# Performance work log

Hardware: AMD Instinct MI355X
Metric: run time of the kernel (lower is better)

Reference implementation:

```python
import jax, jax.numpy as jnp
import numpy as np

N = 100000       # nodes
E = 3200000      # edges (avg degree 32)
IN_F = 256
HID = 256
CLS = 64
LN_EPS = 1e-5


def setup_inputs() -> dict:
    key = jax.random.key(0)
    ks = jax.random.split(key, 8)
    features = jax.random.normal(ks[0], (N, IN_F), jnp.float32)
    src = jax.random.randint(ks[1], (E,), 0, N, dtype=jnp.int32)
    dst = jax.random.randint(ks[2], (E,), 0, N, dtype=jnp.int32)
    glorot = lambda k, sh: jax.random.normal(k, sh, jnp.float32) * np.float32(1.0 / np.sqrt(sh[0]))
    return {
        "features": features, "src": src, "dst": dst,
        "W0": glorot(ks[3], (IN_F, HID)), "b0": jnp.zeros((HID,), jnp.float32),
        "W1": glorot(ks[4], (HID, HID)), "b1": jnp.zeros((HID,), jnp.float32),
        "W2": glorot(ks[5], (HID, CLS)), "b2": jnp.zeros((CLS,), jnp.float32),
    }


def _degrees(src, dst):
    ones = jnp.ones(src.shape[0], jnp.float32)
    deg_out = jnp.maximum(jax.ops.segment_sum(ones, src, num_segments=N), 1.0)
    deg_in = jnpmax = jnp.maximum(jax.ops.segment_sum(ones, dst, num_segments=N), 1.0)
    return deg_out ** -0.5, deg_in ** -0.5


def _graph_conv(h, src, dst, norm_src, norm_dst, W, b, act):
    # DGL GraphConv, norm='both': D_dst^{-1/2} A D_src^{-1/2} X W + b
    h = h * norm_src[:, None]
    agg = jax.ops.segment_sum(h[src], dst, num_segments=N)  # [N, d] scatter-add
    h = agg * norm_dst[:, None]
    h = h @ W + b
    return act(h) if act is not None else h


def _full_layernorm(h):
    # F.layer_norm(h, h.shape): normalize over the ENTIRE tensor, no affine
    mu = jnp.mean(h)
    var = jnp.mean(jnp.square(h - mu))
    return (h - mu) * jax.lax.rsqrt(var + LN_EPS)


def reference(features, src, dst, W0, b0, W1, b1, W2, b2):
    norm_src, norm_dst = _degrees(src, dst)
    h = _graph_conv(features, src, dst, norm_src, norm_dst, W0, b0, jax.nn.relu)
    h = _full_layernorm(h)
    # dropout p=0.0 -> identity
    h = _graph_conv(h, src, dst, norm_src, norm_dst, W1, b1, jax.nn.relu)
    h = _full_layernorm(h)
    h = _graph_conv(h, src, dst, norm_src, norm_dst, W2, b2, None)
    return h
```

## Files before the change

kernel.cpp:

```cpp
#include <hip/hip_runtime.h>
#include <hip/hip_fp16.h>


typedef __attribute__((ext_vector_type(8))) short short8v;
typedef __attribute__((ext_vector_type(4))) float float4v;

struct alignas(8) h4_t { __half2 lo, hi; };

static __device__ __forceinline__ unsigned short f2bf(float x) {
  unsigned int u = __float_as_uint(x);
  unsigned int r = (u + 0x7fffu + ((u >> 16) & 1u)) >> 16;
  return (unsigned short)r;
}
static __device__ __forceinline__ float bf2f(unsigned short h) {
  return __uint_as_float((unsigned int)h << 16);
}
static __device__ __forceinline__ unsigned int f2h2(float a, float b) {
  __half2 h = __floats2half2_rn(a, b);
  return *(unsigned int*)&h;
}
static __device__ __forceinline__ unsigned int bfpack(float a, float b) {
  return (unsigned int)f2bf(a) | ((unsigned int)f2bf(b) << 16);
}

__global__ __launch_bounds__(256) void degrees_k(const int* __restrict__ src,
                                                 const int* __restrict__ dst,
                                                 int* __restrict__ degO,
                                                 int* __restrict__ degI, int E) {
  int e = blockIdx.x * 256 + threadIdx.x;
  if (e < E) {
    atomicAdd(&degO[src[e]], 1);
    atomicAdd(&degI[dst[e]], 1);
  }
}

__global__ __launch_bounds__(256) void norm_k(const int* __restrict__ degO,
                                              const int* __restrict__ degI,
                                              float* __restrict__ ns,
                                              float* __restrict__ nd, int N) {
  int n = blockIdx.x * 256 + threadIdx.x;
  if (n < N) {
    int o = degO[n]; if (o < 1) o = 1;
    int i = degI[n]; if (i < 1) i = 1;
    ns[n] = rsqrtf((float)o);
    nd[n] = rsqrtf((float)i);
  }
}

__global__ __launch_bounds__(256) void scan1_k(const int* __restrict__ in,
                                               int* __restrict__ out,
                                               int* __restrict__ partials, int n) {
  __shared__ int sh[256];
  int t = threadIdx.x;
  int base = blockIdx.x * 2048 + t * 8;
  int v[8];
  int local = 0;
#pragma unroll
  for (int j = 0; j < 8; ++j) {
    int idx = base + j;
    v[j] = (idx < n) ? in[idx] : 0;
    local += v[j];
  }
  sh[t] = local;
  __syncthreads();
  int x = local;
  for (int off = 1; off < 256; off <<= 1) {
    int y = (t >= off) ? sh[t - off] : 0;
    __syncthreads();
    x += y;
    sh[t] = x;
    __syncthreads();
  }
  if (t == 255) partials[blockIdx.x] = x;
  int run = x - local;
#pragma unroll
  for (int j = 0; j < 8; ++j) {
    int idx = base + j;
    if (idx < n) out[idx] = run;
    run += v[j];
  }
}

__global__ void scan2_k(int* partials, int nb) {
  if (threadIdx.x == 0 && blockIdx.x == 0) {
    int run = 0;
    for (int i = 0; i < nb; ++i) { int t = partials[i]; partials[i] = run; run += t; }
  }
}

__global__ __launch_bounds__(256) void scan3_k(int* __restrict__ row_start,
                                               int* __restrict__ cursor,
                                               const int* __restrict__ partials,
                                               int n, int total) {
  int i = blockIdx.x * 256 + threadIdx.x;
  if (i < n) {
    int val = row_start[i] + partials[i >> 11];
    row_start[i] = val;
    cursor[i] = val;
  }
  if (i == 0) row_start[n] = total;
}

__global__ __launch_bounds__(256) void fill_k(const int* __restrict__ src,
                                              const int* __restrict__ dst,
                                              int* __restrict__ cursor,
                                              int* __restrict__ edge_src, int E) {
  int e = blockIdx.x * 256 + threadIdx.x;
  if (e < E) {
    int d = dst[e];
    int pos = atomicAdd(&cursor[d], 1);
    edge_src[pos] = src[e];
  }
}

__global__ __launch_bounds__(256) void prepw_k(const float* __restrict__ W,
                                               unsigned short* __restrict__ Whi,
                                               unsigned short* __restrict__ Wlo,
                                               int K, int csh) {
  int C = 1 << csh;
  int idx = blockIdx.x * 256 + threadIdx.x;
  if (idx >= K * C) return;
  int k = idx >> csh, c = idx & (C - 1);
  float x = W[idx];
  unsigned short h = f2bf(x);
  Whi[c * K + k] = h;
  Wlo[c * K + k] = f2bf(x - bf2f(h));
}

__global__ __launch_bounds__(256) void prescale_h_k(const float* __restrict__ X,
                                                    const float* __restrict__ ns,
                                                    __half* __restrict__ Ah, int N) {
  size_t q = (size_t)blockIdx.x * 256 + threadIdx.x;
  if (q >= (size_t)N * 32) return;
  int row = (int)(q >> 5);
  float s = ns[row];
  float4 v0 = ((const float4*)X)[q * 2];
  float4 v1 = ((const float4*)X)[q * 2 + 1];
  uint4 o;
  o.x = f2h2(v0.x * s, v0.y * s);
  o.y = f2h2(v0.z * s, v0.w * s);
  o.z = f2h2(v1.x * s, v1.y * s);
  o.w = f2h2(v1.z * s, v1.w * s);
  ((uint4*)Ah)[q] = o;
}

__global__ __launch_bounds__(256) void normp_h_k(const float* __restrict__ A,
                                                 const float* __restrict__ ns,
                                                 const double* __restrict__ stats,
                                                 double inv_count,
                                                 __half* __restrict__ Ah, int N) {
  size_t q = (size_t)blockIdx.x * 256 + threadIdx.x;
  if (q >= (size_t)N * 32) return;
  double mu = stats[0] * inv_count;
  double var = stats[1] * inv_count - mu * mu;
  float muf = (float)mu;
  float inv = (float)(1.0 / sqrt(var + 1e-5));
  int row = (int)(q >> 5);
  float sc = ns[row] * inv;
  float4 v0 = ((const float4*)A)[q * 2];
  float4 v1 = ((const float4*)A)[q * 2 + 1];
  uint4 o;
  o.x = f2h2((v0.x - muf) * sc, (v0.y - muf) * sc);
  o.y = f2h2((v0.z - muf) * sc, (v0.w - muf) * sc);
  o.z = f2h2((v1.x - muf) * sc, (v1.y - muf) * sc);
  o.w = f2h2((v1.z - muf) * sc, (v1.w - muf) * sc);
  ((uint4*)Ah)[q] = o;
}

__global__ __launch_bounds__(256) void normp_p_k(const float* __restrict__ A,
                                                 const float* __restrict__ ns,
                                                 const double* __restrict__ stats,
                                                 double inv_count,
                                                 unsigned short* __restrict__ Phi,
                                                 unsigned short* __restrict__ Plo,
                                                 int N) {
  size_t q = (size_t)blockIdx.x * 256 + threadIdx.x;
  if (q >= (size_t)N * 32) return;
  double mu = stats[0] * inv_count;
  double var = stats[1] * inv_count - mu * mu;
  float muf = (float)mu;
  float inv = (float)(1.0 / sqrt(var + 1e-5));
  int row = (int)(q >> 5);
  float sc = ns[row] * inv;
  float x[8];
  float4 v0 = ((const float4*)A)[q * 2];
  float4 v1 = ((const float4*)A)[q * 2 + 1];
  x[0] = (v0.x - muf) * sc; x[1] = (v0.y - muf) * sc;
  x[2] = (v0.z - muf) * sc; x[3] = (v0.w - muf) * sc;
  x[4] = (v1.x - muf) * sc; x[5] = (v1.y - muf) * sc;
  x[6] = (v1.z - muf) * sc; x[7] = (v1.w - muf) * sc;
  uint4 hv, lv;
  unsigned short h;
  float r;
#define SPLIT2(dst_h, dst_l, a, b)                    \
  { unsigned short ha = f2bf(a); float ra = (a) - bf2f(ha);  \
    unsigned short hb = f2bf(b); float rb = (b) - bf2f(hb);  \
    dst_h = (unsigned int)ha | ((unsigned int)hb << 16);     \
    dst_l = (unsigned int)f2bf(ra) | ((unsigned int)f2bf(rb) << 16); }
  SPLIT2(hv.x, lv.x, x[0], x[1]);
  SPLIT2(hv.y, lv.y, x[2], x[3]);
  SPLIT2(hv.z, lv.z, x[4], x[5]);
  SPLIT2(hv.w, lv.w, x[6], x[7]);
#undef SPLIT2
  (void)h; (void)r;
  ((uint4*)Phi)[q] = hv;
  ((uint4*)Plo)[q] = lv;
}

__global__ __launch_bounds__(256) void spmm256_h_k(const __half* __restrict__ Ah,
                                                   const int* __restrict__ rs,
                                                   const int* __restrict__ es,
                                                   const float* __restrict__ nd,
                                                   unsigned short* __restrict__ Bhi,
                                                   unsigned short* __restrict__ Blo,
                                                   int N) {
  int w = (blockIdx.x * 256 + threadIdx.x) >> 6;
  int lane = threadIdx.x & 63;
  if (w >= N) return;
  int s = rs[w], e = rs[w + 1];
  float4 a0 = make_float4(0.f, 0.f, 0.f, 0.f);
  float4 a1 = a0, a2 = a0, a3 = a0;
  int i = s;
  for (; i + 4 <= e; i += 4) {
    int i0 = es[i], i1 = es[i + 1], i2 = es[i + 2], i3 = es[i + 3];
    h4_t v0 = ((const h4_t*)(Ah + (size_t)i0 * 256))[lane];
    h4_t v1 = ((const h4_t*)(Ah + (size_t)i1 * 256))[lane];
    h4_t v2 = ((const h4_t*)(Ah + (size_t)i2 * 256))[lane];
    h4_t v3 = ((const h4_t*)(Ah + (size_t)i3 * 256))[lane];
    float2 f;
    f = __half22float2(v0.lo); a0.x += f.x; a0.y += f.y;
    f = __half22float2(v0.hi); a0.z += f.x; a0.w += f.y;
    f = __half22float2(v1.lo); a1.x += f.x; a1.y += f.y;
    f = __half22float2(v1.hi); a1.z += f.x; a1.w += f.y;
    f = __half22float2(v2.lo); a2.x += f.x; a2.y += f.y;
    f = __half22float2(v2.hi); a2.z += f.x; a2.w += f.y;
    f = __half22float2(v3.lo); a3.x += f.x; a3.y += f.y;
    f = __half22float2(v3.hi); a3.z += f.x; a3.w += f.y;
  }
  for (; i < e; ++i) {
    h4_t v0 = ((const h4_t*)(Ah + (size_t)es[i] * 256))[lane];
    float2 f;
    f = __half22float2(v0.lo); a0.x += f.x; a0.y += f.y;
    f = __half22float2(v0.hi); a0.z += f.x; a0.w += f.y;
  }
  float fd = nd[w];
  float r0 = (a0.x + a1.x + a2.x + a3.x) * fd;
  float r1 = (a0.y + a1.y + a2.y + a3.y) * fd;
  float r2 = (a0.z + a1.z + a2.z + a3.z) * fd;
  float r3 = (a0.w + a1.w + a2.w + a3.w) * fd;
  ushort4 rh, rl;
  rh.x = f2bf(r0); rl.x = f2bf(r0 - bf2f(rh.x));
  rh.y = f2bf(r1); rl.y = f2bf(r1 - bf2f(rh.y));
  rh.z = f2bf(r2); rl.z = f2bf(r2 - bf2f(rh.z));
  rh.w = f2bf(r3); rl.w = f2bf(r3 - bf2f(rh.w));
  *(ushort4*)(Bhi + (size_t)w * 256 + lane * 4) = rh;
  *(ushort4*)(Blo + (size_t)w * 256 + lane * 4) = rl;
}

__global__ __launch_bounds__(256) void spmm64_h_k(const __half* __restrict__ Gh,
                                                  const int* __restrict__ rs,
                                                  const int* __restrict__ es,
                                                  const float* __restrict__ nd,
                                                  const float* __restrict__ b2,
                                                  float* __restrict__ out, int N) {
  int w = (blockIdx.x * 256 + threadIdx.x) >> 6;
  int lane = threadIdx.x & 63;
  if (w >= N) return;
  int s = rs[w], e = rs[w + 1];
  float a0 = 0.f, a1 = 0.f, a2 = 0.f, a3 = 0.f;
  float a4 = 0.f, a5 = 0.f, a6 = 0.f, a7 = 0.f;
  int i = s;
  for (; i + 8 <= e; i += 8) {
    a0 += __half2float(Gh[(size_t)es[i] * 64 + lane]);
    a1 += __half2float(Gh[(size_t)es[i + 1] * 64 + lane]);
    a2 += __half2float(Gh[(size_t)es[i + 2] * 64 + lane]);
    a3 += __half2float(Gh[(size_t)es[i + 3] * 64 + lane]);
    a4 += __half2float(Gh[(size_t)es[i + 4] * 64 + lane]);
    a5 += __half2float(Gh[(size_t)es[i + 5] * 64 + lane]);
    a6 += __half2float(Gh[(size_t)es[i + 6] * 64 + lane]);
    a7 += __half2float(Gh[(size_t)es[i + 7] * 64 + lane]);
  }
  for (; i < e; ++i) a0 += __half2float(Gh[(size_t)es[i] * 64 + lane]);
  float t = ((a0 + a1) + (a2 + a3)) + ((a4 + a5) + (a6 + a7));
  out[(size_t)w * 64 + lane] = t * nd[w] + b2[lane];
}

template <bool EPI, bool OUTH>
__global__ __launch_bounds__(256) void gemm_k(const unsigned short* __restrict__ Ahi,
                                              const unsigned short* __restrict__ Alo,
                                              const unsigned short* __restrict__ Whi,
                                              const unsigned short* __restrict__ Wlo,
                                              const float* __restrict__ bias,
                                              float* __restrict__ Out,
                                              __half* __restrict__ OutH,
                                              int n_rows, int n_cols,
                                              double* __restrict__ stats) {
  __shared__ unsigned short Ahs[64][40];
  __shared__ unsigned short Als[64][40];
  __shared__ unsigned short Hs[64][40];
  __shared__ unsigned short Ls[64][40];
  __shared__ float red0[4], red1[4];
  const int tid = threadIdx.x;
  const int wv = tid >> 6, lane = tid & 63;
  const int r16 = lane & 15, kg = lane >> 4;
  const int m0 = blockIdx.x * 64, n0 = blockIdx.y * 64;
  const int srow = tid >> 2;
  const int sk = (tid & 3) * 8;
  const bool srow_ok = (m0 + srow) < n_rows;
  const unsigned short* ahp = Ahi + (size_t)(m0 + srow) * 256 + sk;
  const unsigned short* alp = Alo + (size_t)(m0 + srow) * 256 + sk;
  const unsigned short* hp = Whi + (size_t)(n0 + srow) * 256 + sk;
  const unsigned short* lp = Wlo + (size_t)(n0 + srow) * 256 + sk;
  float4v acc[4] = {};
  for (int k0 = 0; k0 < 256; k0 += 32) {
    uint4 za = make_uint4(0, 0, 0, 0), zl = za;
    if (srow_ok) {
      za = *(const uint4*)(ahp + k0);
      zl = *(const uint4*)(alp + k0);
    }
    uint4 h4 = *(const uint4*)(hp + k0);
    uint4 l4 = *(const uint4*)(lp + k0);
    *(uint4*)&Ahs[srow][sk] = za;
    *(uint4*)&Als[srow][sk] = zl;
    *(uint4*)&Hs[srow][sk] = h4;
    *(uint4*)&Ls[srow][sk] = l4;
    __syncthreads();
    short8v ahi = *(const short8v*)&Ahs[16 * wv + r16][8 * kg];
    short8v alo = *(const short8v*)&Als[16 * wv + r16][8 * kg];
#pragma unroll
    for (int t = 0; t < 4; ++t) {
      short8v bhi = *(const short8v*)&Hs[16 * t + r16][8 * kg];
      short8v blo = *(const short8v*)&Ls[16 * t + r16][8 * kg];
      acc[t] = __builtin_amdgcn_mfma_f32_16x16x32_bf16(ahi, bhi, acc[t], 0, 0, 0);
      acc[t] = __builtin_amdgcn_mfma_f32_16x16x32_bf16(ahi, blo, acc[t], 0, 0, 0);
      acc[t] = __builtin_amdgcn_mfma_f32_16x16x32_bf16(alo, bhi, acc[t], 0, 0, 0);
    }
    __syncthreads();
  }
  float lsum = 0.f, lsq = 0.f;
#pragma unroll
  for (int t = 0; t < 4; ++t) {
    int col = n0 + 16 * t + r16;
    float b = EPI ? bias[col] : 0.f;
#pragma unroll
    for (int j = 0; j < 4; ++j) {
      int row = m0 + 16 * wv + 4 * kg + j;
      if (row < n_rows) {
        float v = acc[t][j];
        if (EPI) {
          v += b;
          v = v > 0.f ? v : 0.f;
          lsum += v;
          lsq += v * v;
        }
        if (OUTH) OutH[(size_t)row * n_cols + col] = __float2half(v);
        else      Out[(size_t)row * n_cols + col] = v;
      }
    }
  }
  if (EPI) {
#pragma unroll
    for (int off = 32; off > 0; off >>= 1) {
      lsum += __shfl_down(lsum, off, 64);
      lsq += __shfl_down(lsq, off, 64);
    }
    if (lane == 0) { red0[wv] = lsum; red1[wv] = lsq; }
    __syncthreads();
    if (tid == 0) {
      double s = 0.0, q = 0.0;
#pragma unroll
      for (int i = 0; i < 4; ++i) { s += (double)red0[i]; q += (double)red1[i]; }
      atomicAdd(stats, s);
      atomicAdd(stats + 1, q);
    }
  }
}

extern "C" void kernel_launch(void* const* d_in, const int* in_sizes, int n_in,
                              void* d_out, int out_size, void* d_ws, size_t ws_size,
                              hipStream_t stream) {
  const float* features = (const float*)d_in[0];
  const int* src = (const int*)d_in[1];
  const int* dst = (const int*)d_in[2];
  const float* W0 = (const float*)d_in[3];
  const float* b0 = (const float*)d_in[4];
  const float* W1 = (const float*)d_in[5];
  const float* b1 = (const float*)d_in[6];
  const float* W2 = (const float*)d_in[7];
  const float* b2 = (const float*)d_in[8];
  float* out = (float*)d_out;

  const int N = in_sizes[0] / 256;
  const int E = in_sizes[1];

  char* ws = (char*)d_ws;
  const size_t szPlane = (size_t)N * 256 * 2;
  const size_t szR = 2 * szPlane;
  char* R1 = ws;
  char* R2 = ws + szR;
  size_t offEdge = 2 * szR;
  size_t offRow = offEdge + (size_t)E * 4;
  size_t offCur = offRow + ((size_t)N + 1) * 4;
  size_t offDegO = offCur + (size_t)N * 4;
  size_t offDegI = offDegO + (size_t)N * 4;
  size_t offNs = offDegI + (size_t)N * 4;
  size_t offNd = offNs + (size_t)N * 4;
  size_t offPart = offNd + (size_t)N * 4;
  size_t offStats = (offPart + 64 * 4 + 15) & ~(size_t)15;
  size_t offW = (offStats + 4 * sizeof(double) + 15) & ~(size_t)15;
  size_t offWh0 = offW;
  size_t offWl0 = offWh0 + 256 * 256 * 2;
  size_t offWh1 = offWl0 + 256 * 256 * 2;
  size_t offWl1 = offWh1 + 256 * 256 * 2;
  size_t offWh2 = offWl1 + 256 * 256 * 2;
  size_t offWl2 = offWh2 + 256 * 64 * 2;

  int* edge_src = (int*)(ws + offEdge);
  int* row_start = (int*)(ws + offRow);
  int* cursor = (int*)(ws + offCur);
  int* degO = (int*)(ws + offDegO);
  int* degI = (int*)(ws + offDegI);
  float* ns = (float*)(ws + offNs);
  float* nd = (float*)(ws + offNd);
  int* partials = (int*)(ws + offPart);
  double* stats = (double*)(ws + offStats);
  unsigned short* Wh0 = (unsigned short*)(ws + offWh0);
  unsigned short* Wl0 = (unsigned short*)(ws + offWl0);
  unsigned short* Wh1 = (unsigned short*)(ws + offWh1);
  unsigned short* Wl1 = (unsigned short*)(ws + offWl1);
  unsigned short* Wh2 = (unsigned short*)(ws + offWh2);
  unsigned short* Wl2 = (unsigned short*)(ws + offWl2);

  __half* Ah0 = (__half*)R1;
  unsigned short* Bhi0 = (unsigned short*)R2;
  unsigned short* Blo0 = Bhi0 + (size_t)N * 256;
  float* A0 = (float*)R1;
  __half* Ah1 = (__half*)R2;
  unsigned short* Bhi1 = (unsigned short*)R1;
  unsigned short* Blo1 = Bhi1 + (size_t)N * 256;
  float* A1 = (float*)R2;
  unsigned short* A2hi = (unsigned short*)R1;
  unsigned short* A2lo = A2hi + (size_t)N * 256;
  __half* Gh = (__half*)R2;

  const int eb = (E + 255) / 256;
  const int nb = (N + 255) / 256;
  const int sb = (N + 2047) / 2048;
  const int hq = (N * 32 + 255) / 256;
  const int wb = (N + 3) / 4;
  const int gx = (N + 63) / 64;
  const double inv_count = 1.0 / ((double)N * 256.0);

  hipMemsetAsync(degO, 0, (size_t)N * 8, stream);
  hipMemsetAsync(stats, 0, 4 * sizeof(double), stream);

  prepw_k<<<256, 256, 0, stream>>>(W0, Wh0, Wl0, 256, 8);
  prepw_k<<<256, 256, 0, stream>>>(W1, Wh1, Wl1, 256, 8);
  prepw_k<<<64, 256, 0, stream>>>(W2, Wh2, Wl2, 256, 6);

  degrees_k<<<eb, 256, 0, stream>>>(src, dst, degO, degI, E);
  norm_k<<<nb, 256, 0, stream>>>(degO, degI, ns, nd, N);
  scan1_k<<<sb, 256, 0, stream>>>(degI, row_start, partials, N);
  scan2_k<<<1, 64, 0, stream>>>(partials, sb);
  scan3_k<<<nb, 256, 0, stream>>>(row_start, cursor, partials, N, E);
  fill_k<<<eb, 256, 0, stream>>>(src, dst, cursor, edge_src, E);

  prescale_h_k<<<hq, 256, 0, stream>>>(features, ns, Ah0, N);
  spmm256_h_k<<<wb, 256, 0, stream>>>(Ah0, row_start, edge_src, nd, Bhi0, Blo0, N);
  gemm_k<true, false><<<dim3(gx, 4), 256, 0, stream>>>(Bhi0, Blo0, Wh0, Wl0, b0,
                                                       A0, nullptr, N, 256, stats);
  normp_h_k<<<hq, 256, 0, stream>>>(A0, ns, stats, inv_count, Ah1, N);

  spmm256_h_k<<<wb, 256, 0, stream>>>(Ah1, row_start, edge_src, nd, Bhi1, Blo1, N);
  gemm_k<true, false><<<dim3(gx, 4), 256, 0, stream>>>(Bhi1, Blo1, Wh1, Wl1, b1,
                                                       A1, nullptr, N, 256, stats + 2);
  normp_p_k<<<hq, 256, 0, stream>>>(A1, ns, stats + 2, inv_count, A2hi, A2lo, N);

  gemm_k<false, true><<<dim3(gx, 1), 256, 0, stream>>>(A2hi, A2lo, Wh2, Wl2, nullptr,
                                                       nullptr, Gh, N, 64, nullptr);
  spmm64_h_k<<<wb, 256, 0, stream>>>(Gh, row_start, edge_src, nd, b2, out, N);
}
```

Baseline: 1.683 ms.

## Build CSR via two-level bucketed counting sort instead of per-node atomics

Replaces the per-destination degree atomics, three-kernel scan and global-atomic fill with a bucketed counting sort. Edges are first histogrammed into buckets of 128 destinations in shared memory, then scattered as (src,dst) pairs into bucket order. A per-bucket block then builds row_start, in-degrees and edge_src with shared-memory atomics. This aims to cut contended global atomics and random scatters, at the cost of an extra 8-byte-per-edge pass through a temporary buffer and a serial single-thread bucket scan over roughly 782 buckets.

```diff
diff --git a/kernel.cpp b/kernel.cpp
--- a/kernel.cpp
+++ b/kernel.cpp
@@ -4,6 +4,8 @@
 
 typedef __attribute__((ext_vector_type(8))) short short8v;
 typedef __attribute__((ext_vector_type(4))) float float4v;
+
+#define NBSH 7
 
 struct alignas(8) h4_t { __half2 lo, hi; };
 
@@ -19,18 +21,90 @@
   __half2 h = __floats2half2_rn(a, b);
   return *(unsigned int*)&h;
 }
-static __device__ __forceinline__ unsigned int bfpack(float a, float b) {
-  return (unsigned int)f2bf(a) | ((unsigned int)f2bf(b) << 16);
-}
-
-__global__ __launch_bounds__(256) void degrees_k(const int* __restrict__ src,
-                                                 const int* __restrict__ dst,
-                                                 int* __restrict__ degO,
-                                                 int* __restrict__ degI, int E) {
+
+__global__ __launch_bounds__(256) void passA_k(const int* __restrict__ src,
+                                               const int* __restrict__ dst,
+                                               int* __restrict__ degO,
+                                               int* __restrict__ bucketCnt,
+                                               int E, int nbuck) {
+  extern __shared__ int lh[];
+  for (int i = threadIdx.x; i < nbuck; i += 256) lh[i] = 0;
+  __syncthreads();
+  int stride = gridDim.x * 256;
+  for (int e = blockIdx.x * 256 + threadIdx.x; e < E; e += stride) {
+    atomicAdd(&degO[src[e]], 1);
+    atomicAdd(&lh[dst[e] >> NBSH], 1);
+  }
+  __syncthreads();
+  for (int i = threadIdx.x; i < nbuck; i += 256)
+    if (lh[i]) atomicAdd(&bucketCnt[i], lh[i]);
+}
+
+__global__ void scanB_k(const int* __restrict__ bucketCnt,
+                        int* __restrict__ bucketStart,
+                        int* __restrict__ bucketCur,
+                        int* __restrict__ row_start,
+                        int nbuck, int N, int E) {
+  if (threadIdx.x == 0 && blockIdx.x == 0) {
+    int run = 0;
+    for (int i = 0; i < nbuck; ++i) {
+      bucketStart[i] = run;
+      bucketCur[i] = run;
+      run += bucketCnt[i];
+    }
+    bucketStart[nbuck] = run;
+    row_start[N] = E;
+  }
+}
+
+__global__ __launch_bounds__(256) void passB_k(const int* __restrict__ src,
+                                               const int* __restrict__ dst,
+                                               int* __restrict__ bucketCur,
+                                               unsigned long long* __restrict__ pairs,
+                                               int E) {
   int e = blockIdx.x * 256 + threadIdx.x;
   if (e < E) {
-    atomicAdd(&degO[src[e]], 1);
-    atomicAdd(&degI[dst[e]], 1);
+    int d = dst[e];
+    int pos = atomicAdd(&bucketCur[d >> NBSH], 1);
+    pairs[pos] = (unsigned long long)(unsigned int)src[e] |
+                 ((unsigned long long)(unsigned int)d << 32);
+  }
+}
+
+__global__ __launch_bounds__(256) void passC_k(const unsigned long long* __restrict__ pairs,
+                                               const int* __restrict__ bucketStart,
+                                               int* __restrict__ row_start,
+                                               int* __restrict__ degI,
+                                               int* __restrict__ edge_src, int N) {
+  __shared__ int hist[128], cur[128];
+  int b = blockIdx.x;
+  int base = bucketStart[b], cnt = bucketStart[b + 1] - base;
+  int dstBase = b << NBSH;
+  int nloc = N - dstBase; if (nloc > 128) nloc = 128;
+  int t = threadIdx.x;
+  if (t < 128) hist[t] = 0;
+  __syncthreads();
+  for (int i = t; i < cnt; i += 256) {
+    int d = (int)(pairs[base + i] >> 32);
+    atomicAdd(&hist[d & 127], 1);
+  }
+  __syncthreads();
+  if (t == 0) {
+    int run = base;
+    for (int j = 0; j < 128; ++j) { cur[j] = run; run += hist[j]; }
+  }
+  __syncthreads();
+  if (t < nloc) {
+    row_start[dstBase + t] = cur[t];
+    degI[dstBase + t] = hist[t];
+  }
+  __syncthreads();
+  for (int i = t; i < cnt; i += 256) {
+    unsigned long long p = pairs[base + i];
+    int s = (int)(p & 0xffffffffull);
+    int d = (int)(p >> 32);
+    int pos = atomicAdd(&cur[d & 127], 1);
+    edge_src[pos] = s;
   }
 }
 
@@ -44,72 +118,6 @@
     int i = degI[n]; if (i < 1) i = 1;
     ns[n] = rsqrtf((float)o);
     nd[n] = rsqrtf((float)i);
-  }
-}
-
-__global__ __launch_bounds__(256) void scan1_k(const int* __restrict__ in,
-                                               int* __restrict__ out,
-                                               int* __restrict__ partials, int n) {
-  __shared__ int sh[256];
-  int t = threadIdx.x;
-  int base = blockIdx.x * 2048 + t * 8;
-  int v[8];
-  int local = 0;
-#pragma unroll
-  for (int j = 0; j < 8; ++j) {
-    int idx = base + j;
-    v[j] = (idx < n) ? in[idx] : 0;
-    local += v[j];
-  }
-  sh[t] = local;
-  __syncthreads();
-  int x = local;
-  for (int off = 1; off < 256; off <<= 1) {
-    int y = (t >= off) ? sh[t - off] : 0;
-    __syncthreads();
-    x += y;
-    sh[t] = x;
-    __syncthreads();
-  }
-  if (t == 255) partials[blockIdx.x] = x;
-  int run = x - local;
-#pragma unroll
-  for (int j = 0; j < 8; ++j) {
-    int idx = base + j;
-    if (idx < n) out[idx] = run;
-    run += v[j];
-  }
-}
-
-__global__ void scan2_k(int* partials, int nb) {
-  if (threadIdx.x == 0 && blockIdx.x == 0) {
-    int run = 0;
-    for (int i = 0; i < nb; ++i) { int t = partials[i]; partials[i] = run; run += t; }
-  }
-}
-
-__global__ __launch_bounds__(256) void scan3_k(int* __restrict__ row_start,
-                                               int* __restrict__ cursor,
-                                               const int* __restrict__ partials,
-                                               int n, int total) {
-  int i = blockIdx.x * 256 + threadIdx.x;
-  if (i < n) {
-    int val = row_start[i] + partials[i >> 11];
-    row_start[i] = val;
-    cursor[i] = val;
-  }
-  if (i == 0) row_start[n] = total;
-}
-
-__global__ __launch_bounds__(256) void fill_k(const int* __restrict__ src,
-                                              const int* __restrict__ dst,
-                                              int* __restrict__ cursor,
-                                              int* __restrict__ edge_src, int E) {
-  int e = blockIdx.x * 256 + threadIdx.x;
-  if (e < E) {
-    int d = dst[e];
-    int pos = atomicAdd(&cursor[d], 1);
-    edge_src[pos] = src[e];
   }
 }
 
@@ -190,8 +198,6 @@
   x[4] = (v1.x - muf) * sc; x[5] = (v1.y - muf) * sc;
   x[6] = (v1.z - muf) * sc; x[7] = (v1.w - muf) * sc;
   uint4 hv, lv;
-  unsigned short h;
-  float r;
 #define SPLIT2(dst_h, dst_l, a, b)                    \
   { unsigned short ha = f2bf(a); float ra = (a) - bf2f(ha);  \
     unsigned short hb = f2bf(b); float rb = (b) - bf2f(hb);  \
@@ -202,7 +208,6 @@
   SPLIT2(hv.z, lv.z, x[4], x[5]);
   SPLIT2(hv.w, lv.w, x[6], x[7]);
 #undef SPLIT2
-  (void)h; (void)r;
   ((uint4*)Phi)[q] = hv;
   ((uint4*)Plo)[q] = lv;
 }
@@ -392,6 +397,7 @@
 
   const int N = in_sizes[0] / 256;
   const int E = in_sizes[1];
+  const int nbuck = (N + 127) >> 7;
 
   char* ws = (char*)d_ws;
   const size_t szPlane = (size_t)N * 256 * 2;
@@ -400,13 +406,14 @@
   char* R2 = ws + szR;
   size_t offEdge = 2 * szR;
   size_t offRow = offEdge + (size_t)E * 4;
-  size_t offCur = offRow + ((size_t)N + 1) * 4;
-  size_t offDegO = offCur + (size_t)N * 4;
+  size_t offDegO = offRow + ((size_t)N + 1) * 4;
   size_t offDegI = offDegO + (size_t)N * 4;
   size_t offNs = offDegI + (size_t)N * 4;
   size_t offNd = offNs + (size_t)N * 4;
-  size_t offPart = offNd + (size_t)N * 4;
-  size_t offStats = (offPart + 64 * 4 + 15) & ~(size_t)15;
+  size_t offBC = offNd + (size_t)N * 4;
+  size_t offBS = offBC + ((size_t)nbuck + 1) * 4;
+  size_t offBU = offBS + ((size_t)nbuck + 1) * 4;
+  size_t offStats = (offBU + ((size_t)nbuck + 1) * 4 + 15) & ~(size_t)15;
   size_t offW = (offStats + 4 * sizeof(double) + 15) & ~(size_t)15;
   size_t offWh0 = offW;
   size_t offWl0 = offWh0 + 256 * 256 * 2;
@@ -417,12 +424,13 @@
 
   int* edge_src = (int*)(ws + offEdge);
   int* row_start = (int*)(ws + offRow);
-  int* cursor = (int*)(ws + offCur);
   int* degO = (int*)(ws + offDegO);
   int* degI = (int*)(ws + offDegI);
   float* ns = (float*)(ws + offNs);
   float* nd = (float*)(ws + offNd);
-  int* partials = (int*)(ws + offPart);
+  int* bucketCnt = (int*)(ws + offBC);
+  int* bucketStart = (int*)(ws + offBS);
+  int* bucketCur = (int*)(ws + offBU);
   double* stats = (double*)(ws + offStats);
   unsigned short* Wh0 = (unsigned short*)(ws + offWh0);
   unsigned short* Wl0 = (unsigned short*)(ws + offWl0);
@@ -430,6 +438,8 @@
   unsigned short* Wl1 = (unsigned short*)(ws + offWl1);
   unsigned short* Wh2 = (unsigned short*)(ws + offWh2);
   unsigned short* Wl2 = (unsigned short*)(ws + offWl2);
+
+  unsigned long long* pairs = (unsigned long long*)R2;
 
   __half* Ah0 = (__half*)R1;
   unsigned short* Bhi0 = (unsigned short*)R2;
@@ -445,25 +455,26 @@
 
   const int eb = (E + 255) / 256;
   const int nb = (N + 255) / 256;
-  const int sb = (N + 2047) / 2048;
   const int hq = (N * 32 + 255) / 256;
   const int wb = (N + 3) / 4;
   const int gx = (N + 63) / 64;
   const double inv_count = 1.0 / ((double)N * 256.0);
 
-  hipMemsetAsync(degO, 0, (size_t)N * 8, stream);
+  hipMemsetAsync(degO, 0, (size_t)N * 4, stream);
+  hipMemsetAsync(bucketCnt, 0, ((size_t)nbuck + 1) * 4, stream);
   hipMemsetAsync(stats, 0, 4 * sizeof(double), stream);
 
   prepw_k<<<256, 256, 0, stream>>>(W0, Wh0, Wl0, 256, 8);
   prepw_k<<<256, 256, 0, stream>>>(W1, Wh1, Wl1, 256, 8);
   prepw_k<<<64, 256, 0, stream>>>(W2, Wh2, Wl2, 256, 6);
 
-  degrees_k<<<eb, 256, 0, stream>>>(src, dst, degO, degI, E);
+  passA_k<<<1024, 256, nbuck * 4, stream>>>(src, dst, degO, bucketCnt, E, nbuck);
+  scanB_k<<<1, 64, 0, stream>>>(bucketCnt, bucketStart, bucketCur, row_start,
+                                nbuck, N, E);
+  passB_k<<<eb, 256, 0, stream>>>(src, dst, bucketCur, pairs, E);
+  passC_k<<<nbuck, 256, 0, stream>>>(pairs, bucketStart, row_start, degI,
+                                     edge_src, N);
   norm_k<<<nb, 256, 0, stream>>>(degO, degI, ns, nd, N);
-  scan1_k<<<sb, 256, 0, stream>>>(degI, row_start, partials, N);
-  scan2_k<<<1, 64, 0, stream>>>(partials, sb);
-  scan3_k<<<nb, 256, 0, stream>>>(row_start, cursor, partials, N, E);
-  fill_k<<<eb, 256, 0, stream>>>(src, dst, cursor, edge_src, E);
 
   prescale_h_k<<<hq, 256, 0, stream>>>(features, ns, Ah0, N);
   spmm256_h_k<<<wb, 256, 0, stream>>>(Ah0, row_start, edge_src, nd, Bhi0, Blo0, N);
```

After: 2.133 ms. 1.27x slower.
